# Performance work log

Measured on AMD Instinct MI355X. Metric: run time of the kernel, lower is better.

Reference implementation:

```python
import jax, jax.numpy as jnp
import numpy as np

B, Q, P, H, NH, NKV, D = 8, 16, 4096, 4096, 32, 8, 128
ROPE_BASE = 10000.0


def setup_inputs() -> dict:
    key = jax.random.key(0)
    ks = jax.random.split(key, 8)
    hidden_states = jax.random.normal(ks[0], (B, Q, H), dtype=jnp.float32)
    past_key = jax.random.normal(ks[1], (B, NKV, P, D), dtype=jnp.float32)
    past_value = jax.random.normal(ks[2], (B, NKV, P, D), dtype=jnp.float32)
    # draft tokens continue right after the cached prefix
    position_ids = jnp.broadcast_to(P + jnp.arange(Q, dtype=jnp.int64), (B, Q))
    attention_bias = jnp.zeros((B, 1, Q, P + Q), dtype=jnp.float32)
    s = 0.02
    Wq = jax.random.normal(ks[3], (H, NH * D), dtype=jnp.float32) * s
    Wk = jax.random.normal(ks[4], (H, NKV * D), dtype=jnp.float32) * s
    Wv = jax.random.normal(ks[5], (H, NKV * D), dtype=jnp.float32) * s
    Wo = jax.random.normal(ks[6], (NH * D, H), dtype=jnp.float32) * s
    return {"hidden_states": hidden_states, "position_ids": position_ids,
            "past_key": past_key, "past_value": past_value,
            "attention_bias": attention_bias, "Wq": Wq, "Wk": Wk, "Wv": Wv, "Wo": Wo}


def _rope_cos_sin(position_ids, dtype):
    # inv_freq over even dims, GPT-NeoX layout: angles repeated (concat) over halves
    inv_freq = 1.0 / (ROPE_BASE ** (jnp.arange(0, D, 2, dtype=jnp.float32) / D))
    ang = position_ids.astype(jnp.float32)[:, :, None] * inv_freq  # [B,Q,D/2]
    emb = jnp.concatenate([ang, ang], axis=-1)  # [B,Q,D]
    cos = jnp.cos(emb).astype(dtype)[:, None, :, :]  # [B,1,Q,D]
    sin = jnp.sin(emb).astype(dtype)[:, None, :, :]
    return cos, sin


def _rotate_half(x):
    x1, x2 = jnp.split(x, 2, axis=-1)
    return jnp.concatenate([-x2, x1], axis=-1)


def reference(hidden_states, position_ids, past_key, past_value, attention_bias,
              Wq, Wk, Wv, Wo):
    b, q_len, _ = hidden_states.shape
    n_kv = past_key.shape[1]
    groups = NH // n_kv
    # projections
    q = (hidden_states @ Wq).reshape(b, q_len, NH, D).transpose(0, 2, 1, 3)   # [B,NH,Q,D]
    k = (hidden_states @ Wk).reshape(b, q_len, n_kv, D).transpose(0, 2, 1, 3)  # [B,NKV,Q,D]
    v = (hidden_states @ Wv).reshape(b, q_len, n_kv, D).transpose(0, 2, 1, 3)
    # RoPE
    cos, sin = _rope_cos_sin(position_ids, hidden_states.dtype)
    q = q * cos + _rotate_half(q) * sin
    k = k * cos + _rotate_half(k) * sin
    # KV-cache append
    k_all = jnp.concatenate([past_key, k], axis=2)    # [B,NKV,S,D]
    v_all = jnp.concatenate([past_value, v], axis=2)
    # GQA attention: group query heads per kv head instead of repeat_interleave
    qg = q.reshape(b, n_kv, groups, q_len, D)
    scale = 1.0 / jnp.sqrt(jnp.asarray(D, dtype=hidden_states.dtype))
    scores = jnp.einsum('bkgqd,bksd->bkgqs', qg, k_all) * scale
    scores = scores + attention_bias[:, :, None, :, :]  # bias [B,1,Q,S] -> broadcast
    probs = jax.nn.softmax(scores, axis=-1)
    out = jnp.einsum('bkgqs,bksd->bkgqd', probs, v_all)  # [B,NKV,G,Q,D]
    out = out.reshape(b, NH, q_len, D).transpose(0, 2, 1, 3).reshape(b, q_len, NH * D)
    return out @ Wo
```

## Files before the change

### kernel.cpp

```cpp
#include <hip/hip_runtime.h>
#include <hip/hip_bf16.h>

#define NB 8
#define NQ 16
#define NP 4096
#define NHID 4096
#define NHEADS 32
#define NKVH 8
#define NG 4
#define ND 128
#define NM 128
#define NSEQ 4112
#define N_QKV 6144
#define SPLITK 8
#define NS 16

typedef __attribute__((ext_vector_type(8))) short bf16x8;
typedef __attribute__((ext_vector_type(4))) float f32x4;

__device__ __forceinline__ unsigned short f2bf(float f) {
  unsigned int u = __float_as_uint(f);
  u = (u + 0x7FFFu + ((u >> 16) & 1u)) >> 16;
  return (unsigned short)u;
}

__device__ __forceinline__ unsigned cvtpk(float lo, float hi) {
  unsigned r;
  asm("v_cvt_pk_bf16_f32 %0, %1, %2" : "=v"(r) : "v"(lo), "v"(hi));
  return r;
}

__device__ __forceinline__ float bf2f(unsigned short u) {
  return __uint_as_float(((unsigned)u) << 16);
}

#define TRREAD(dst, a32) \
  asm volatile("ds_read_b64_tr_b16 %0, %1" : "=v"(dst) : "v"(a32))
#define LGKM0() asm volatile("s_waitcnt lgkmcnt(0)" ::: "memory")
#define SBAR()                              \
  do {                                      \
    __builtin_amdgcn_sched_barrier(0);      \
    __builtin_amdgcn_s_barrier();           \
    __builtin_amdgcn_sched_barrier(0);      \
  } while (0)

__global__ __launch_bounds__(256) void k_cvt(const float* __restrict__ x,
                                             unsigned short* __restrict__ y, int n4) {
  int i = blockIdx.x * 256 + threadIdx.x;
  if (i >= n4) return;
  f32x4 v = ((const f32x4*)x)[i];
  uint2 o;
  o.x = cvtpk(v[0], v[1]);
  o.y = cvtpk(v[2], v[3]);
  ((uint2*)y)[i] = o;
}

template<int CT>
__global__ __launch_bounds__(256) void k_gemm(
    const unsigned short* __restrict__ A, int lda,
    const float* __restrict__ W0, const float* __restrict__ W1,
    const float* __restrict__ W2, int nw0, int nw1, int N, int KS,
    float* __restrict__ part) {
  constexpr int BN = CT * 32;
  constexpr int NT = CT * 2;
  constexpr int NW4 = BN / 4;
  constexpr int KST = 256 / NW4;
  __shared__ __align__(16) char Bl[8 * NT * 128];
  int n0 = blockIdx.x * BN;
  int k0 = blockIdx.y * KS;
  const float* Wp; int ldw, ncol;
  if (n0 < nw0)      { Wp = W0; ldw = nw0;       ncol = n0; }
  else if (n0 < nw1) { Wp = W1; ldw = nw1 - nw0; ncol = n0 - nw0; }
  else               { Wp = W2; ldw = N - nw1;   ncol = n0 - nw1; }
  int tid = threadIdx.x, lane = tid & 63, wid = tid >> 6;
  int r16 = lane & 15, hi = lane >> 4;
  int wr = wid >> 1, wc = wid & 1;
  int n4 = tid & (NW4 - 1), krow = tid / NW4;
  unsigned lb = (unsigned)(uintptr_t)(void*)Bl;

  f32x4 acc[4][CT];
#pragma unroll
  for (int i = 0; i < 4; ++i)
#pragma unroll
    for (int j = 0; j < CT; ++j) acc[i][j] = {0.f, 0.f, 0.f, 0.f};

  f32x4 cur[CT], nxt[CT];
#pragma unroll
  for (int r = 0; r < CT; ++r) {
    cur[r] = *(const f32x4*)&Wp[(size_t)(k0 + krow + r * KST) * ldw + ncol + n4 * 4];
    nxt[r] = cur[r];
  }

  for (int kk = 0; kk < KS; kk += 32) {
    SBAR();
    if (kk + 32 < KS) {
#pragma unroll
      for (int r = 0; r < CT; ++r)
        nxt[r] = *(const f32x4*)&Wp[(size_t)(k0 + kk + 32 + krow + r * KST) * ldw + ncol + n4 * 4];
    }
#pragma unroll
    for (int r = 0; r < CT; ++r) {
      int k = krow + r * KST;
      uint2 u;
      u.x = cvtpk(cur[r][0], cur[r][1]);
      u.y = cvtpk(cur[r][2], cur[r][3]);
      *(uint2*)(Bl + ((k >> 2) * NT + (n4 >> 2)) * 128 + (k & 3) * 32 + (n4 & 3) * 8) = u;
    }
    LGKM0();
    SBAR();
    bf16x8 af[4];
#pragma unroll
    for (int rt = 0; rt < 4; ++rt)
      af[rt] = *(const bf16x8*)&A[(size_t)(wr * 64 + rt * 16 + r16) * lda + k0 + kk + hi * 8];
    unsigned long long rr[2 * CT];
#pragma unroll
    for (int ct = 0; ct < CT; ++ct) {
      int s1 = hi * (2 * NT) + wc * CT + ct;
      TRREAD(rr[ct * 2],     lb + s1 * 128 + r16 * 8);
      TRREAD(rr[ct * 2 + 1], lb + (s1 + NT) * 128 + r16 * 8);
    }
    LGKM0();
    __builtin_amdgcn_sched_barrier(0);
    __builtin_amdgcn_s_setprio(1);
#pragma unroll
    for (int ct = 0; ct < CT; ++ct) {
      union { unsigned long long u[2]; bf16x8 v; } cc;
      cc.u[0] = rr[ct * 2]; cc.u[1] = rr[ct * 2 + 1];
#pragma unroll
      for (int rt = 0; rt < 4; ++rt)
        acc[rt][ct] = __builtin_amdgcn_mfma_f32_16x16x32_bf16(af[rt], cc.v, acc[rt][ct], 0, 0, 0);
    }
    __builtin_amdgcn_s_setprio(0);
#pragma unroll
    for (int r = 0; r < CT; ++r) cur[r] = nxt[r];
  }
  float* po = part + (size_t)blockIdx.y * NM * N;
#pragma unroll
  for (int rt = 0; rt < 4; ++rt)
#pragma unroll
    for (int ct = 0; ct < CT; ++ct)
#pragma unroll
      for (int r = 0; r < 4; ++r) {
        int m = wr * 64 + rt * 16 + hi * 4 + r;
        int n = n0 + wc * CT * 16 + ct * 16 + r16;
        po[(size_t)m * N + n] = acc[rt][ct][r];
      }
}

__global__ __launch_bounds__(256) void k_rope(
    const float* __restrict__ part, const void* __restrict__ posv,
    unsigned short* __restrict__ qb, unsigned short* __restrict__ kb,
    unsigned short* __restrict__ vb) {
  int t = blockIdx.x * 256 + threadIdx.x;
  int d = t & 63;
  int rest = t >> 6;
  int h = rest % 48;
  int m = rest / 48;
  if (m >= NM) return;
  const int* p32 = (const int*)posv;
  const long long* p64 = (const long long*)posv;
  bool is64 = (p64[0] == (long long)p32[0]);
  int pos = is64 ? (int)p64[m] : p32[m];
  int b = m >> 4, q = m & 15;

  int c1, c2;
  if (h < 32)      { c1 = h * ND + d; }
  else if (h < 40) { c1 = NHID + (h - 32) * ND + d; }
  else             { c1 = NHID + 1024 + (h - 40) * ND + d; }
  c2 = c1 + 64;
  float x1 = 0.f, x2 = 0.f;
#pragma unroll
  for (int c = 0; c < SPLITK; ++c) {
    x1 += part[((size_t)c * NM + m) * N_QKV + c1];
    x2 += part[((size_t)c * NM + m) * N_QKV + c2];
  }
  if (h < 40) {
    float invf = __expf(-(float)d * 0.14391156831212787f);
    float th = (float)pos * invf;
    float cs = cosf(th), sn = sinf(th);
    float o1 = x1 * cs - x2 * sn;
    float o2 = x2 * cs + x1 * sn;
    if (h < 32) {
      o1 *= 0.08838834764831845f;
      o2 *= 0.08838834764831845f;
      int kv = h >> 2, g = h & 3;
      size_t base = ((((size_t)b * NKVH + kv) * NG + g) * NQ + q) * ND;
      qb[base + d] = f2bf(o1);
      qb[base + d + 64] = f2bf(o2);
    } else {
      int kvh = h - 32;
      size_t base = (((size_t)b * NKVH + kvh) * NQ + q) * ND;
      kb[base + d] = f2bf(o1);
      kb[base + d + 64] = f2bf(o2);
    }
  } else {
    int kvh = h - 40;
    size_t base = (((size_t)b * NKVH + kvh) * NQ + q) * ND;
    vb[base + d] = f2bf(x1);
    vb[base + d + 64] = f2bf(x2);
  }
}

template<int NSPL>
__global__ __launch_bounds__(256, 2) void k_attn(
    const unsigned short* __restrict__ qb, const unsigned short* __restrict__ kb,
    const unsigned short* __restrict__ vb, const float* __restrict__ pastK,
    const float* __restrict__ pastV, const float* __restrict__ bias,
    unsigned short* __restrict__ pout, float* __restrict__ pml) {
  __shared__ __align__(16) char lds[40960];
  char* Pl = lds + 32768;
  constexpr int KEYS = NP / NSPL;
  constexpr int NSUB = KEYS / 32;
  int bkv = blockIdx.x;
  int split = blockIdx.y;
  int b = bkv >> 3, kv = bkv & 7;
  int tid = threadIdx.x, lane = tid & 63, wid = tid >> 6;
  int r16 = lane & 15, hi = lane >> 4;

  const unsigned short* qbase = qb + ((((size_t)b * NKVH + kv) * NG + wid) * NQ) * ND;
  bf16x8 qf[4];
#pragma unroll
  for (int kd = 0; kd < 4; ++kd)
    qf[kd] = *(const bf16x8*)&qbase[r16 * ND + kd * 32 + hi * 8];

  float m_run[4], l_lane[4];
  f32x4 oacc[8];
#pragma unroll
  for (int r = 0; r < 4; ++r) { m_run[r] = -1e30f; l_lane[r] = 0.f; }
#pragma unroll
  for (int dt = 0; dt < 8; ++dt) oacc[dt] = {0.f, 0.f, 0.f, 0.f};

  int s0 = split * KEYS;
  const float* Kg = pastK + ((size_t)(b * NKVH + kv) * NP + s0) * ND;
  const float* Vg = pastV + ((size_t)(b * NKVH + kv) * NP + s0) * ND;
  const float* biasrow = bias + (size_t)(b * NQ) * NSEQ;
  int d4 = tid & 31, sr = tid >> 5;
  bool last = (split == NSPL - 1);

  f32x4 rwK[4], rwV[4];
  float br0, br1, bt[4];
  bf16x8 tk, tv;

  auto kissue = [&](int tile) {
    const float* Kn = Kg + (size_t)tile * 32 * ND;
#pragma unroll
    for (int it = 0; it < 4; ++it)
      rwK[it] = *(const f32x4*)&Kn[(size_t)(sr + it * 8) * ND + d4 * 4];
  };
  auto vissue = [&](int tile) {
    const float* Vn = Vg + (size_t)tile * 32 * ND;
#pragma unroll
    for (int it = 0; it < 4; ++it)
      rwV[it] = *(const f32x4*)&Vn[(size_t)(sr + it * 8) * ND + d4 * 4];
  };
  auto bissue = [&](int tile) {
    {
      int e = tid;        int q = e >> 5, j = e & 31;
      br0 = biasrow[(size_t)q * NSEQ + s0 + tile * 32 + j];
    }
    {
      int e = 256 + tid;  int q = e >> 5, j = e & 31;
      br1 = biasrow[(size_t)q * NSEQ + s0 + tile * 32 + j];
    }
  };
  auto kconv = [&](char* Kl) {
#pragma unroll
    for (int it = 0; it < 4; ++it) {
      int s = sr + it * 8;
      uint2 u;
      u.x = cvtpk(rwK[it][0], rwK[it][1]); u.y = cvtpk(rwK[it][2], rwK[it][3]);
      *(uint2*)(Kl + s * 256 + ((d4 * 8) ^ ((s & 7) << 4))) = u;
    }
  };
  auto vconv = [&](char* Vl) {
#pragma unroll
    for (int it = 0; it < 4; ++it) {
      int s = sr + it * 8;
      uint2 u;
      u.x = cvtpk(rwV[it][0], rwV[it][1]); u.y = cvtpk(rwV[it][2], rwV[it][3]);
      *(uint2*)(Vl + ((s >> 2) * 8 + (d4 >> 2)) * 128 + (s & 3) * 32 + (d4 & 3) * 8) = u;
    }
  };
  auto bstore = [&](char* Bb) {
    {
      int e = tid;        int q = e >> 5, j = e & 31;
      *(float*)(Bb + q * 128 + ((j * 4) ^ ((q & 7) << 4))) = br0;
    }
    {
      int e = 256 + tid;  int q = e >> 5, j = e & 31;
      *(float*)(Bb + q * 128 + ((j * 4) ^ ((q & 7) << 4))) = br1;
    }
  };

  f32x4 sc[2];
  auto qk_softmax = [&](char* Kl, char* Bb, bool tail) {
    __builtin_amdgcn_s_setprio(1);
#pragma unroll
    for (int ct = 0; ct < 2; ++ct) {
      f32x4 a = {0.f, 0.f, 0.f, 0.f};
      int s = ct * 16 + r16;
#pragma unroll
      for (int kd = 0; kd < 4; ++kd) {
        bf16x8 kf = *(const bf16x8*)(Kl + s * 256 + ((kd * 64 + hi * 16) ^ ((s & 7) << 4)));
        a = __builtin_amdgcn_mfma_f32_16x16x32_bf16(qf[kd], kf, a, 0, 0, 0);
      }
      sc[ct] = a;
    }
    __builtin_amdgcn_s_setprio(0);
    if (!tail) {
#pragma unroll
      for (int ct = 0; ct < 2; ++ct)
#pragma unroll
        for (int r = 0; r < 4; ++r) {
          int q = hi * 4 + r, j = ct * 16 + r16;
          sc[ct][r] += *(const float*)(Bb + q * 128 + ((j * 4) ^ ((q & 7) << 4)));
        }
    } else {
#pragma unroll
      for (int ct = 0; ct < 2; ++ct)
#pragma unroll
        for (int r = 0; r < 4; ++r) {
          if (ct == 0) sc[ct][r] += bt[r];
          else         sc[ct][r] = -1e30f;
        }
    }
    float pmax[4];
#pragma unroll
    for (int r = 0; r < 4; ++r)
      pmax[r] = fmaxf(sc[0][r], sc[1][r]);
    bool ok = (pmax[0] <= m_run[0] + 8.f) && (pmax[1] <= m_run[1] + 8.f) &&
              (pmax[2] <= m_run[2] + 8.f) && (pmax[3] <= m_run[3] + 8.f);
    if (!__all(ok)) {
#pragma unroll
      for (int r = 0; r < 4; ++r) {
        float v = pmax[r];
        v = fmaxf(v, __shfl_xor(v, 1));
        v = fmaxf(v, __shfl_xor(v, 2));
        v = fmaxf(v, __shfl_xor(v, 4));
        v = fmaxf(v, __shfl_xor(v, 8));
        float mnew = fmaxf(m_run[r], v);
        float fac = __expf(m_run[r] - mnew);
        m_run[r] = mnew;
        l_lane[r] *= fac;
#pragma unroll
        for (int dt = 0; dt < 8; ++dt) oacc[dt][r] *= fac;
      }
    }
#pragma unroll
    for (int ct = 0; ct < 2; ++ct)
#pragma unroll
      for (int r = 0; r < 4; ++r) {
        float p = __expf(sc[ct][r] - m_run[r]);
        l_lane[r] += p;
        int q = hi * 4 + r, j2 = ct * 16 + r16;
        *(unsigned short*)(Pl + wid * 1024 + q * 64 + ((j2 * 2) ^ ((q & 3) << 4))) = f2bf(p);
      }
  };

  auto pv = [&](char* Vl) {
    unsigned vb32 = (unsigned)(uintptr_t)(void*)Vl;
    bf16x8 pa = *(const bf16x8*)(Pl + wid * 1024 + r16 * 64 +
                                 ((hi * 16) ^ ((r16 & 3) << 4)));
#pragma unroll
    for (int dh = 0; dh < 2; ++dh) {
      unsigned long long rr[8];
#pragma unroll
      for (int dq = 0; dq < 4; ++dq) {
        int sA = hi * 16 + dh * 4 + dq;
        TRREAD(rr[dq * 2],     vb32 + sA * 128 + r16 * 8);
        TRREAD(rr[dq * 2 + 1], vb32 + (sA + 8) * 128 + r16 * 8);
      }
      LGKM0();
      __builtin_amdgcn_sched_barrier(0);
      __builtin_amdgcn_s_setprio(1);
#pragma unroll
      for (int dq = 0; dq < 4; ++dq) {
        union { unsigned long long u[2]; bf16x8 v; } cc;
        cc.u[0] = rr[dq * 2]; cc.u[1] = rr[dq * 2 + 1];
        oacc[dh * 4 + dq] = __builtin_amdgcn_mfma_f32_16x16x32_bf16(pa, cc.v, oacc[dh * 4 + dq], 0, 0, 0);
      }
      __builtin_amdgcn_s_setprio(0);
    }
  };

  kissue(0);
  vissue(0);
  bissue(0);
  kconv(lds + 0);
  vconv(lds + 16384);
  bstore(lds + 36864);
  LGKM0();

  int cur = 0;
  for (int sub = 0; sub < NSUB; ++sub) {
    char* KlC = lds + cur * 8192;
    char* VlC = lds + 16384 + cur * 8192;
    char* BbC = lds + 36864 + cur * 2048;
    char* KlN = lds + (cur ^ 1) * 8192;
    char* VlN = lds + 16384 + (cur ^ 1) * 8192;
    char* BbN = lds + 36864 + (cur ^ 1) * 2048;
    SBAR();
    bool pf = (sub + 1 < NSUB);
    if (pf) {
      kissue(sub + 1);
      bissue(sub + 1);
    } else if (last) {
      int s = tid >> 4, d8 = tid & 15;
      const unsigned short* Kn = kb + (((size_t)b * NKVH + kv) * NQ) * ND;
      const unsigned short* Vn = vb + (((size_t)b * NKVH + kv) * NQ) * ND;
      tk = *(const bf16x8*)&Kn[s * ND + d8 * 8];
      tv = *(const bf16x8*)&Vn[s * ND + d8 * 8];
#pragma unroll
      for (int r = 0; r < 4; ++r)
        bt[r] = biasrow[(size_t)(hi * 4 + r) * NSEQ + NP + r16];
    }
    qk_softmax(KlC, BbC, false);
    if (pf) {
      kconv(KlN);
      vissue(sub + 1);
    } else if (last) {
      int s = tid >> 4, d8 = tid & 15;
      *(bf16x8*)(KlN + s * 256 + ((d8 * 16) ^ ((s & 7) << 4))) = tk;
    }
    pv(VlC);
    if (pf) {
      vconv(VlN);
      bstore(BbN);
    } else if (last) {
      int s = tid >> 4, d8 = tid & 15;
      *(bf16x8*)(VlN + ((s >> 2) * 8 + (d8 >> 1)) * 128 + (s & 3) * 32 + (d8 & 1) * 16) = tv;
    }
    LGKM0();
    if (pf || last) cur ^= 1;
  }
  if (last) {
    SBAR();
    qk_softmax(lds + cur * 8192, (char*)0, true);
    pv(lds + 16384 + cur * 8192);
  }

  float l_run[4];
#pragma unroll
  for (int r = 0; r < 4; ++r) {
    float s = l_lane[r];
    s += __shfl_xor(s, 1);
    s += __shfl_xor(s, 2);
    s += __shfl_xor(s, 4);
    s += __shfl_xor(s, 8);
    l_run[r] = s;
  }
  SBAR();
  char* My = lds + wid * 4096;
#pragma unroll
  for (int dt = 0; dt < 8; ++dt)
#pragma unroll
    for (int r = 0; r < 4; ++r)
      *(unsigned short*)(My + (hi * 4 + r) * 256 + (dt * 16 + r16) * 2) = f2bf(oacc[dt][r]);
  LGKM0();
  const int NROW = NB * NKVH * NG * NQ;
  size_t rowbase = ((size_t)(b * NKVH + kv) * NG + wid) * NQ;
  unsigned short* po = pout + ((size_t)split * NROW + rowbase) * ND;
#pragma unroll
  for (int it = 0; it < 4; ++it) {
    int row = it * 4 + (lane >> 4);
    uint4 vv = *(uint4*)(My + row * 256 + r16 * 16);
    *(uint4*)&po[(size_t)row * ND + r16 * 8] = vv;
  }
  if (r16 == 0) {
#pragma unroll
    for (int r = 0; r < 4; ++r) {
      size_t idx = ((size_t)split * NROW + rowbase + hi * 4 + r) * 2;
      pml[idx] = m_run[r];
      pml[idx + 1] = l_run[r];
    }
  }
}

template<int NSPL>
__global__ __launch_bounds__(256) void k_combine(
    const unsigned short* __restrict__ pout, const float* __restrict__ pml,
    unsigned short* __restrict__ Aatt) {
  const int NROW = NB * NKVH * NG * NQ;
  int row = blockIdx.x * 2 + (threadIdx.x >> 7);
  int d = threadIdx.x & 127;
  float mv[NSPL], lv[NSPL];
  float M = -1e30f;
#pragma unroll
  for (int c = 0; c < NSPL; ++c) {
    mv[c] = pml[((size_t)c * NROW + row) * 2];
    lv[c] = pml[((size_t)c * NROW + row) * 2 + 1];
    M = fmaxf(M, mv[c]);
  }
  float L = 0.f, acc = 0.f;
#pragma unroll
  for (int c = 0; c < NSPL; ++c) {
    float w = __expf(mv[c] - M);
    L += lv[c] * w;
    acc += bf2f(pout[((size_t)c * NROW + row) * ND + d]) * w;
  }
  float o = acc / L;
  int q = row & 15, g = (row >> 4) & 3, kvh = (row >> 6) & 7, b = row >> 9;
  Aatt[(size_t)(b * NQ + q) * NHID + (kvh * NG + g) * ND + d] = f2bf(o);
}

__global__ __launch_bounds__(256) void k_red(const float* __restrict__ part,
                                             float* __restrict__ out) {
  int i = blockIdx.x * 256 + threadIdx.x;
  float s = 0.f;
#pragma unroll
  for (int c = 0; c < SPLITK; ++c) s += part[(size_t)c * (NM * NHID) + i];
  out[i] = s;
}

extern "C" void kernel_launch(void* const* d_in, const int* in_sizes, int n_in,
                              void* d_out, int out_size, void* d_ws, size_t ws_size,
                              hipStream_t stream) {
  const float* hidden = (const float*)d_in[0];
  const void* pos = d_in[1];
  const float* pastK = (const float*)d_in[2];
  const float* pastV = (const float*)d_in[3];
  const float* bias = (const float*)d_in[4];
  const float* Wq = (const float*)d_in[5];
  const float* Wk = (const float*)d_in[6];
  const float* Wv = (const float*)d_in[7];
  const float* Wo = (const float*)d_in[8];
  float* out = (float*)d_out;

  char* ws = (char*)d_ws;
  size_t off = 0;
  auto alloc = [&](size_t bytes) {
    char* p = ws + off;
    off += (bytes + 255) & ~(size_t)255;
    return p;
  };
  unsigned short* hb   = (unsigned short*)alloc((size_t)NM * NHID * 2);
  unsigned short* qb   = (unsigned short*)alloc((size_t)NB * NKVH * NG * NQ * ND * 2);
  unsigned short* kb   = (unsigned short*)alloc((size_t)NB * NKVH * NQ * ND * 2);
  unsigned short* vb   = (unsigned short*)alloc((size_t)NB * NKVH * NQ * ND * 2);
  unsigned short* Aatt = (unsigned short*)alloc((size_t)NM * NHID * 2);

  size_t ml16 = (size_t)16 * 8192 * 2 * 4;
  size_t po16 = (size_t)16 * 8192 * ND * 2;
  size_t partB = (size_t)SPLITK * NM * N_QKV * 4;
  size_t need16 = (ml16 + po16 > partB) ? ml16 + po16 : partB;
  int NSP = (ws_size >= off + need16 + 4096) ? 16 : 8;
  float* pml = (float*)(ws + off);
  unsigned short* pout = (unsigned short*)(ws + off + (NSP == 16 ? ml16 : ml16 / 2));
  float* part = (float*)(ws + off);

  k_cvt<<<512, 256, 0, stream>>>(hidden, hb, NM * NHID / 4);
  k_gemm<2><<<dim3(96, SPLITK), 256, 0, stream>>>(hb, NHID, Wq, Wk, Wv, 4096, 5120,
                                                  N_QKV, NHID / SPLITK, part);
  k_rope<<<1536, 256, 0, stream>>>(part, pos, qb, kb, vb);
  if (NSP == 16) {
    k_attn<16><<<dim3(64, 16), 256, 0, stream>>>(qb, kb, vb, pastK, pastV, bias, pout, pml);
    k_combine<16><<<4096, 256, 0, stream>>>(pout, pml, Aatt);
  } else {
    k_attn<8><<<dim3(64, 8), 256, 0, stream>>>(qb, kb, vb, pastK, pastV, bias, pout, pml);
    k_combine<8><<<4096, 256, 0, stream>>>(pout, pml, Aatt);
  }
  k_gemm<2><<<dim3(64, SPLITK), 256, 0, stream>>>(Aatt, NHID, Wo, Wo, Wo, 4096, 8192,
                                                  NHID, NHID / SPLITK, part);
  k_red<<<2048, 256, 0, stream>>>(part, out);
}
```

Baseline: 154.2 us.

## Prefetch K and bias two tiles ahead with ping-pong register sets

K tiles and bias rows are now loaded into global-memory registers two sub-tiles ahead, alternating between two register sets (A/B). V loads are issued at the start of each iteration, which gives them more time to land before conversion. The loop is fully unrolled so the buffer parity is a compile-time constant. This aims to hide more global-load latency, at the cost of extra VGPRs that may reduce occupancy.

```diff
diff --git a/kernel.cpp b/kernel.cpp
--- a/kernel.cpp
+++ b/kernel.cpp
@@ -13,7 +13,6 @@
 #define NSEQ 4112
 #define N_QKV 6144
 #define SPLITK 8
-#define NS 16
 
 typedef __attribute__((ext_vector_type(8))) short bf16x8;
 typedef __attribute__((ext_vector_type(4))) float f32x4;
@@ -237,59 +236,78 @@
   int d4 = tid & 31, sr = tid >> 5;
   bool last = (split == NSPL - 1);
 
-  f32x4 rwK[4], rwV[4];
-  float br0, br1, bt[4];
+  f32x4 kRA[4], kRB[4], vR[4];
+  float brA0, brA1, brB0, brB1, bt[4];
   bf16x8 tk, tv;
 
-  auto kissue = [&](int tile) {
+  auto kissueA = [&](int tile) {
     const float* Kn = Kg + (size_t)tile * 32 * ND;
 #pragma unroll
     for (int it = 0; it < 4; ++it)
-      rwK[it] = *(const f32x4*)&Kn[(size_t)(sr + it * 8) * ND + d4 * 4];
+      kRA[it] = *(const f32x4*)&Kn[(size_t)(sr + it * 8) * ND + d4 * 4];
+  };
+  auto kissueB = [&](int tile) {
+    const float* Kn = Kg + (size_t)tile * 32 * ND;
+#pragma unroll
+    for (int it = 0; it < 4; ++it)
+      kRB[it] = *(const f32x4*)&Kn[(size_t)(sr + it * 8) * ND + d4 * 4];
   };
   auto vissue = [&](int tile) {
     const float* Vn = Vg + (size_t)tile * 32 * ND;
 #pragma unroll
     for (int it = 0; it < 4; ++it)
-      rwV[it] = *(const f32x4*)&Vn[(size_t)(sr + it * 8) * ND + d4 * 4];
-  };
-  auto bissue = [&](int tile) {
-    {
-      int e = tid;        int q = e >> 5, j = e & 31;
-      br0 = biasrow[(size_t)q * NSEQ + s0 + tile * 32 + j];
-    }
-    {
-      int e = 256 + tid;  int q = e >> 5, j = e & 31;
-      br1 = biasrow[(size_t)q * NSEQ + s0 + tile * 32 + j];
-    }
-  };
-  auto kconv = [&](char* Kl) {
+      vR[it] = *(const f32x4*)&Vn[(size_t)(sr + it * 8) * ND + d4 * 4];
+  };
+  auto bissueA = [&](int tile) {
+    { int e = tid;       int q = e >> 5, j = e & 31;
+      brA0 = biasrow[(size_t)q * NSEQ + s0 + tile * 32 + j]; }
+    { int e = 256 + tid; int q = e >> 5, j = e & 31;
+      brA1 = biasrow[(size_t)q * NSEQ + s0 + tile * 32 + j]; }
+  };
+  auto bissueB = [&](int tile) {
+    { int e = tid;       int q = e >> 5, j = e & 31;
+      brB0 = biasrow[(size_t)q * NSEQ + s0 + tile * 32 + j]; }
+    { int e = 256 + tid; int q = e >> 5, j = e & 31;
+      brB1 = biasrow[(size_t)q * NSEQ + s0 + tile * 32 + j]; }
+  };
+  auto kconvA = [&](char* Kl) {
 #pragma unroll
     for (int it = 0; it < 4; ++it) {
       int s = sr + it * 8;
       uint2 u;
-      u.x = cvtpk(rwK[it][0], rwK[it][1]); u.y = cvtpk(rwK[it][2], rwK[it][3]);
+      u.x = cvtpk(kRA[it][0], kRA[it][1]); u.y = cvtpk(kRA[it][2], kRA[it][3]);
       *(uint2*)(Kl + s * 256 + ((d4 * 8) ^ ((s & 7) << 4))) = u;
     }
   };
-  auto vconv = [&](char* Vl) {
+  auto kconvB = [&](char* Kl) {
 #pragma unroll
     for (int it = 0; it < 4; ++it) {
       int s = sr + it * 8;
       uint2 u;
-      u.x = cvtpk(rwV[it][0], rwV[it][1]); u.y = cvtpk(rwV[it][2], rwV[it][3]);
+      u.x = cvtpk(kRB[it][0], kRB[it][1]); u.y = cvtpk(kRB[it][2], kRB[it][3]);
+      *(uint2*)(Kl + s * 256 + ((d4 * 8) ^ ((s & 7) << 4))) = u;
+    }
+  };
+  auto vconv = [&](char* Vl) {
+#pragma unroll
+    for (int it = 0; it < 4; ++it) {
+      int s = sr + it * 8;
+      uint2 u;
+      u.x = cvtpk(vR[it][0], vR[it][1]); u.y = cvtpk(vR[it][2], vR[it][3]);
       *(uint2*)(Vl + ((s >> 2) * 8 + (d4 >> 2)) * 128 + (s & 3) * 32 + (d4 & 3) * 8) = u;
     }
   };
-  auto bstore = [&](char* Bb) {
-    {
-      int e = tid;        int q = e >> 5, j = e & 31;
-      *(float*)(Bb + q * 128 + ((j * 4) ^ ((q & 7) << 4))) = br0;
-    }
-    {
-      int e = 256 + tid;  int q = e >> 5, j = e & 31;
-      *(float*)(Bb + q * 128 + ((j * 4) ^ ((q & 7) << 4))) = br1;
-    }
+  auto bstoreA = [&](char* Bb) {
+    { int e = tid;       int q = e >> 5, j = e & 31;
+      *(float*)(Bb + q * 128 + ((j * 4) ^ ((q & 7) << 4))) = brA0; }
+    { int e = 256 + tid; int q = e >> 5, j = e & 31;
+      *(float*)(Bb + q * 128 + ((j * 4) ^ ((q & 7) << 4))) = brA1; }
+  };
+  auto bstoreB = [&](char* Bb) {
+    { int e = tid;       int q = e >> 5, j = e & 31;
+      *(float*)(Bb + q * 128 + ((j * 4) ^ ((q & 7) << 4))) = brB0; }
+    { int e = 256 + tid; int q = e >> 5, j = e & 31;
+      *(float*)(Bb + q * 128 + ((j * 4) ^ ((q & 7) << 4))) = brB1; }
   };
 
   f32x4 sc[2];
@@ -383,28 +401,31 @@
     }
   };
 
-  kissue(0);
+  kissueA(0);
   vissue(0);
-  bissue(0);
-  kconv(lds + 0);
+  bissueA(0);
+  kissueB(1);
+  bissueB(1);
+  kconvA(lds + 0);
   vconv(lds + 16384);
-  bstore(lds + 36864);
+  bstoreA(lds + 36864);
   LGKM0();
 
-  int cur = 0;
+#pragma unroll
   for (int sub = 0; sub < NSUB; ++sub) {
-    char* KlC = lds + cur * 8192;
-    char* VlC = lds + 16384 + cur * 8192;
-    char* BbC = lds + 36864 + cur * 2048;
-    char* KlN = lds + (cur ^ 1) * 8192;
-    char* VlN = lds + 16384 + (cur ^ 1) * 8192;
-    char* BbN = lds + 36864 + (cur ^ 1) * 2048;
+    const int p = sub & 1;
+    char* KlC = lds + p * 8192;
+    char* VlC = lds + 16384 + p * 8192;
+    char* BbC = lds + 36864 + p * 2048;
+    char* KlN = lds + (p ^ 1) * 8192;
+    char* VlN = lds + 16384 + (p ^ 1) * 8192;
+    char* BbN = lds + 36864 + (p ^ 1) * 2048;
     SBAR();
-    bool pf = (sub + 1 < NSUB);
-    if (pf) {
-      kissue(sub + 1);
-      bissue(sub + 1);
-    } else if (last) {
+    if (sub + 1 < NSUB) vissue(sub + 1);
+    if (sub + 2 < NSUB) {
+      if (p == 0) { kissueA(sub + 2); bissueA(sub + 2); }
+      else        { kissueB(sub + 2); bissueB(sub + 2); }
+    } else if (sub + 2 == NSUB && last) {
       int s = tid >> 4, d8 = tid & 15;
       const unsigned short* Kn = kb + (((size_t)b * NKVH + kv) * NQ) * ND;
       const unsigned short* Vn = vb + (((size_t)b * NKVH + kv) * NQ) * ND;
@@ -415,28 +436,26 @@
         bt[r] = biasrow[(size_t)(hi * 4 + r) * NSEQ + NP + r16];
     }
     qk_softmax(KlC, BbC, false);
-    if (pf) {
-      kconv(KlN);
-      vissue(sub + 1);
+    if (sub + 1 < NSUB) {
+      if (p == 0) { kconvB(KlN); bstoreB(BbN); }
+      else        { kconvA(KlN); bstoreA(BbN); }
     } else if (last) {
       int s = tid >> 4, d8 = tid & 15;
       *(bf16x8*)(KlN + s * 256 + ((d8 * 16) ^ ((s & 7) << 4))) = tk;
     }
     pv(VlC);
-    if (pf) {
+    if (sub + 1 < NSUB) {
       vconv(VlN);
-      bstore(BbN);
     } else if (last) {
       int s = tid >> 4, d8 = tid & 15;
       *(bf16x8*)(VlN + ((s >> 2) * 8 + (d8 >> 1)) * 128 + (s & 3) * 32 + (d8 & 1) * 16) = tv;
     }
     LGKM0();
-    if (pf || last) cur ^= 1;
   }
   if (last) {
     SBAR();
-    qk_softmax(lds + cur * 8192, (char*)0, true);
-    pv(lds + 16384 + cur * 8192);
+    qk_softmax(lds + (NSUB & 1) * 8192, (char*)0, true);
+    pv(lds + 16384 + (NSUB & 1) * 8192);
   }
 
   float l_run[4];
```

Measured after the change: 154.6 us. Within noise of the previous version (+0.2%).

## Rework attention so each wave owns a private key range without block barriers

Applied to the files above, without the earlier changes.

The split-KV attention kernel is rebuilt. Each block now serves one query group, and each of its four waves walks its own slice of keys with private LDS buffers for K, V and P, so no block-wide barriers are needed. Bias is loaded straight into registers instead of being staged through LDS. The split count drops to 4 (or 2), giving 16 (or 8) partial slots per row, which matches the existing combine kernel. The cost is that each fp32 K/V tile is now fetched by four blocks (one per group) instead of once per block, so more global or L2 traffic and more registers per wave are traded for removing synchronisation.

```diff
diff --git a/kernel.cpp b/kernel.cpp
--- a/kernel.cpp
+++ b/kernel.cpp
@@ -13,7 +13,6 @@
 #define NSEQ 4112
 #define N_QKV 6144
 #define SPLITK 8
-#define NS 16
 
 typedef __attribute__((ext_vector_type(8))) short bf16x8;
 typedef __attribute__((ext_vector_type(4))) float f32x4;
@@ -202,22 +201,27 @@
 }
 
 template<int NSPL>
-__global__ __launch_bounds__(256, 2) void k_attn(
+__global__ __launch_bounds__(256) void k_attn3(
     const unsigned short* __restrict__ qb, const unsigned short* __restrict__ kb,
     const unsigned short* __restrict__ vb, const float* __restrict__ pastK,
     const float* __restrict__ pastV, const float* __restrict__ bias,
     unsigned short* __restrict__ pout, float* __restrict__ pml) {
-  __shared__ __align__(16) char lds[40960];
-  char* Pl = lds + 32768;
-  constexpr int KEYS = NP / NSPL;
-  constexpr int NSUB = KEYS / 32;
-  int bkv = blockIdx.x;
+  __shared__ __align__(16) char lds[69632];
+  constexpr int RK = NP / NSPL / 4;
+  constexpr int ITER = RK / 32;
+  int g = blockIdx.x & 3, bkv = blockIdx.x >> 2;
   int split = blockIdx.y;
   int b = bkv >> 3, kv = bkv & 7;
   int tid = threadIdx.x, lane = tid & 63, wid = tid >> 6;
   int r16 = lane & 15, hi = lane >> 4;
-
-  const unsigned short* qbase = qb + ((((size_t)b * NKVH + kv) * NG + wid) * NQ) * ND;
+  int lrow = lane >> 2, lq = lane & 3;
+  char* S  = lds + wid * 17408;
+  char* Kl = S;
+  char* Vl = S + 8192;
+  char* Pb = S + 16384;
+  bool tailw = (split == NSPL - 1) && (wid == 3);
+
+  const unsigned short* qbase = qb + ((((size_t)b * NKVH + kv) * NG + g) * NQ) * ND;
   bf16x8 qf[4];
 #pragma unroll
   for (int kd = 0; kd < 4; ++kd)
@@ -230,70 +234,84 @@
 #pragma unroll
   for (int dt = 0; dt < 8; ++dt) oacc[dt] = {0.f, 0.f, 0.f, 0.f};
 
-  int s0 = split * KEYS;
+  int s0 = split * (NP / NSPL) + wid * RK;
   const float* Kg = pastK + ((size_t)(b * NKVH + kv) * NP + s0) * ND;
   const float* Vg = pastV + ((size_t)(b * NKVH + kv) * NP + s0) * ND;
   const float* biasrow = bias + (size_t)(b * NQ) * NSEQ;
-  int d4 = tid & 31, sr = tid >> 5;
-  bool last = (split == NSPL - 1);
-
-  f32x4 rwK[4], rwV[4];
-  float br0, br1, bt[4];
-  bf16x8 tk, tv;
-
-  auto kissue = [&](int tile) {
-    const float* Kn = Kg + (size_t)tile * 32 * ND;
-#pragma unroll
-    for (int it = 0; it < 4; ++it)
-      rwK[it] = *(const f32x4*)&Kn[(size_t)(sr + it * 8) * ND + d4 * 4];
-  };
-  auto vissue = [&](int tile) {
-    const float* Vn = Vg + (size_t)tile * 32 * ND;
-#pragma unroll
-    for (int it = 0; it < 4; ++it)
-      rwV[it] = *(const f32x4*)&Vn[(size_t)(sr + it * 8) * ND + d4 * 4];
-  };
-  auto bissue = [&](int tile) {
-    {
-      int e = tid;        int q = e >> 5, j = e & 31;
-      br0 = biasrow[(size_t)q * NSEQ + s0 + tile * 32 + j];
-    }
-    {
-      int e = 256 + tid;  int q = e >> 5, j = e & 31;
-      br1 = biasrow[(size_t)q * NSEQ + s0 + tile * 32 + j];
-    }
-  };
-  auto kconv = [&](char* Kl) {
-#pragma unroll
-    for (int it = 0; it < 4; ++it) {
-      int s = sr + it * 8;
+
+  f32x4 kLo[8], kHi[8], vLo[8], vHi[8];
+  float br[8], bt[4] = {0.f, 0.f, 0.f, 0.f};
+
+  auto kisL = [&](int t) {
+    const float* P = Kg + (size_t)t * 32 * ND;
+#pragma unroll
+    for (int i = 0; i < 8; ++i)
+      kLo[i] = *(const f32x4*)&P[(size_t)lrow * ND + lq * 32 + i * 4];
+  };
+  auto kisH = [&](int t) {
+    const float* P = Kg + ((size_t)t * 32 + 16) * ND;
+#pragma unroll
+    for (int i = 0; i < 8; ++i)
+      kHi[i] = *(const f32x4*)&P[(size_t)lrow * ND + lq * 32 + i * 4];
+  };
+  auto visL = [&](int t) {
+    const float* P = Vg + (size_t)t * 32 * ND;
+#pragma unroll
+    for (int i = 0; i < 8; ++i)
+      vLo[i] = *(const f32x4*)&P[(size_t)lrow * ND + lq * 32 + i * 4];
+  };
+  auto visH = [&](int t) {
+    const float* P = Vg + ((size_t)t * 32 + 16) * ND;
+#pragma unroll
+    for (int i = 0; i < 8; ++i)
+      vHi[i] = *(const f32x4*)&P[(size_t)lrow * ND + lq * 32 + i * 4];
+  };
+  auto bis = [&](int t) {
+#pragma unroll
+    for (int ct = 0; ct < 2; ++ct)
+#pragma unroll
+      for (int r = 0; r < 4; ++r)
+        br[ct * 4 + r] = biasrow[(size_t)(hi * 4 + r) * NSEQ + s0 + t * 32 + ct * 16 + r16];
+  };
+  auto kcvL = [&]() {
+#pragma unroll
+    for (int i = 0; i < 8; ++i) {
+      int s = lrow, d0 = lq * 32 + i * 4;
       uint2 u;
-      u.x = cvtpk(rwK[it][0], rwK[it][1]); u.y = cvtpk(rwK[it][2], rwK[it][3]);
-      *(uint2*)(Kl + s * 256 + ((d4 * 8) ^ ((s & 7) << 4))) = u;
-    }
-  };
-  auto vconv = [&](char* Vl) {
-#pragma unroll
-    for (int it = 0; it < 4; ++it) {
-      int s = sr + it * 8;
+      u.x = cvtpk(kLo[i][0], kLo[i][1]); u.y = cvtpk(kLo[i][2], kLo[i][3]);
+      *(uint2*)(Kl + s * 256 + ((d0 * 2) ^ ((s & 7) << 4))) = u;
+    }
+  };
+  auto kcvH = [&]() {
+#pragma unroll
+    for (int i = 0; i < 8; ++i) {
+      int s = lrow + 16, d0 = lq * 32 + i * 4;
       uint2 u;
-      u.x = cvtpk(rwV[it][0], rwV[it][1]); u.y = cvtpk(rwV[it][2], rwV[it][3]);
-      *(uint2*)(Vl + ((s >> 2) * 8 + (d4 >> 2)) * 128 + (s & 3) * 32 + (d4 & 3) * 8) = u;
-    }
-  };
-  auto bstore = [&](char* Bb) {
-    {
-      int e = tid;        int q = e >> 5, j = e & 31;
-      *(float*)(Bb + q * 128 + ((j * 4) ^ ((q & 7) << 4))) = br0;
-    }
-    {
-      int e = 256 + tid;  int q = e >> 5, j = e & 31;
-      *(float*)(Bb + q * 128 + ((j * 4) ^ ((q & 7) << 4))) = br1;
+      u.x = cvtpk(kHi[i][0], kHi[i][1]); u.y = cvtpk(kHi[i][2], kHi[i][3]);
+      *(uint2*)(Kl + s * 256 + ((d0 * 2) ^ ((s & 7) << 4))) = u;
+    }
+  };
+  auto vcvL = [&]() {
+#pragma unroll
+    for (int i = 0; i < 8; ++i) {
+      int s = lrow, d0 = lq * 32 + i * 4;
+      uint2 u;
+      u.x = cvtpk(vLo[i][0], vLo[i][1]); u.y = cvtpk(vLo[i][2], vLo[i][3]);
+      *(uint2*)(Vl + ((s >> 2) * 8 + (d0 >> 4)) * 128 + (s & 3) * 32 + (d0 & 15) * 2) = u;
+    }
+  };
+  auto vcvH = [&]() {
+#pragma unroll
+    for (int i = 0; i < 8; ++i) {
+      int s = lrow + 16, d0 = lq * 32 + i * 4;
+      uint2 u;
+      u.x = cvtpk(vHi[i][0], vHi[i][1]); u.y = cvtpk(vHi[i][2], vHi[i][3]);
+      *(uint2*)(Vl + ((s >> 2) * 8 + (d0 >> 4)) * 128 + (s & 3) * 32 + (d0 & 15) * 2) = u;
     }
   };
 
   f32x4 sc[2];
-  auto qk_softmax = [&](char* Kl, char* Bb, bool tail) {
+  auto qk_softmax = [&](bool tail) {
     __builtin_amdgcn_s_setprio(1);
 #pragma unroll
     for (int ct = 0; ct < 2; ++ct) {
@@ -311,10 +329,8 @@
 #pragma unroll
       for (int ct = 0; ct < 2; ++ct)
 #pragma unroll
-        for (int r = 0; r < 4; ++r) {
-          int q = hi * 4 + r, j = ct * 16 + r16;
-          sc[ct][r] += *(const float*)(Bb + q * 128 + ((j * 4) ^ ((q & 7) << 4)));
-        }
+        for (int r = 0; r < 4; ++r)
+          sc[ct][r] += br[ct * 4 + r];
     } else {
 #pragma unroll
       for (int ct = 0; ct < 2; ++ct)
@@ -353,14 +369,13 @@
         float p = __expf(sc[ct][r] - m_run[r]);
         l_lane[r] += p;
         int q = hi * 4 + r, j2 = ct * 16 + r16;
-        *(unsigned short*)(Pl + wid * 1024 + q * 64 + ((j2 * 2) ^ ((q & 3) << 4))) = f2bf(p);
-      }
-  };
-
-  auto pv = [&](char* Vl) {
+        *(unsigned short*)(Pb + q * 64 + ((j2 * 2) ^ ((q & 3) << 4))) = f2bf(p);
+      }
+  };
+
+  auto pv = [&]() {
     unsigned vb32 = (unsigned)(uintptr_t)(void*)Vl;
-    bf16x8 pa = *(const bf16x8*)(Pl + wid * 1024 + r16 * 64 +
-                                 ((hi * 16) ^ ((r16 & 3) << 4)));
+    bf16x8 pa = *(const bf16x8*)(Pb + r16 * 64 + ((hi * 16) ^ ((r16 & 3) << 4)));
 #pragma unroll
     for (int dh = 0; dh < 2; ++dh) {
       unsigned long long rr[8];
@@ -383,60 +398,41 @@
     }
   };
 
-  kissue(0);
-  vissue(0);
-  bissue(0);
-  kconv(lds + 0);
-  vconv(lds + 16384);
-  bstore(lds + 36864);
+  kisL(0); kisH(0); visL(0); visH(0);
+  bis(0);
+  kcvL(); kcvH(); vcvL(); vcvH();
   LGKM0();
 
-  int cur = 0;
-  for (int sub = 0; sub < NSUB; ++sub) {
-    char* KlC = lds + cur * 8192;
-    char* VlC = lds + 16384 + cur * 8192;
-    char* BbC = lds + 36864 + cur * 2048;
-    char* KlN = lds + (cur ^ 1) * 8192;
-    char* VlN = lds + 16384 + (cur ^ 1) * 8192;
-    char* BbN = lds + 36864 + (cur ^ 1) * 2048;
-    SBAR();
-    bool pf = (sub + 1 < NSUB);
-    if (pf) {
-      kissue(sub + 1);
-      bissue(sub + 1);
-    } else if (last) {
-      int s = tid >> 4, d8 = tid & 15;
+  for (int t = 0; t < ITER; ++t) {
+    bool pf = (t + 1 < ITER);
+    if (pf) { kisL(t + 1); kisH(t + 1); visL(t + 1); visH(t + 1); }
+    qk_softmax(false);
+    if (pf) bis(t + 1);
+    if (pf) { kcvL(); kcvH(); }
+    pv();
+    if (pf) { vcvL(); vcvH(); }
+    else if (tailw) {
       const unsigned short* Kn = kb + (((size_t)b * NKVH + kv) * NQ) * ND;
       const unsigned short* Vn = vb + (((size_t)b * NKVH + kv) * NQ) * ND;
-      tk = *(const bf16x8*)&Kn[s * ND + d8 * 8];
-      tv = *(const bf16x8*)&Vn[s * ND + d8 * 8];
+#pragma unroll
+      for (int i = 0; i < 4; ++i) {
+        bf16x8 kk = *(const bf16x8*)&Kn[(size_t)lrow * ND + lq * 32 + i * 8];
+        int db = lq * 64 + i * 16;
+        *(bf16x8*)(Kl + lrow * 256 + (db ^ ((lrow & 7) << 4))) = kk;
+        bf16x8 vv = *(const bf16x8*)&Vn[(size_t)lrow * ND + lq * 32 + i * 8];
+        int d0 = lq * 32 + i * 8;
+        *(bf16x8*)(Vl + ((lrow >> 2) * 8 + (d0 >> 4)) * 128 +
+                   (lrow & 3) * 32 + (d0 & 15) * 2) = vv;
+      }
 #pragma unroll
       for (int r = 0; r < 4; ++r)
         bt[r] = biasrow[(size_t)(hi * 4 + r) * NSEQ + NP + r16];
     }
-    qk_softmax(KlC, BbC, false);
-    if (pf) {
-      kconv(KlN);
-      vissue(sub + 1);
-    } else if (last) {
-      int s = tid >> 4, d8 = tid & 15;
-      *(bf16x8*)(KlN + s * 256 + ((d8 * 16) ^ ((s & 7) << 4))) = tk;
-    }
-    pv(VlC);
-    if (pf) {
-      vconv(VlN);
-      bstore(BbN);
-    } else if (last) {
-      int s = tid >> 4, d8 = tid & 15;
-      *(bf16x8*)(VlN + ((s >> 2) * 8 + (d8 >> 1)) * 128 + (s & 3) * 32 + (d8 & 1) * 16) = tv;
-    }
     LGKM0();
-    if (pf || last) cur ^= 1;
-  }
-  if (last) {
-    SBAR();
-    qk_softmax(lds + cur * 8192, (char*)0, true);
-    pv(lds + 16384 + cur * 8192);
+  }
+  if (tailw) {
+    qk_softmax(true);
+    pv();
   }
 
   float l_run[4];
@@ -449,8 +445,7 @@
     s += __shfl_xor(s, 8);
     l_run[r] = s;
   }
-  SBAR();
-  char* My = lds + wid * 4096;
+  char* My = Kl;
 #pragma unroll
   for (int dt = 0; dt < 8; ++dt)
 #pragma unroll
@@ -458,18 +453,19 @@
       *(unsigned short*)(My + (hi * 4 + r) * 256 + (dt * 16 + r16) * 2) = f2bf(oacc[dt][r]);
   LGKM0();
   const int NROW = NB * NKVH * NG * NQ;
-  size_t rowbase = ((size_t)(b * NKVH + kv) * NG + wid) * NQ;
-  unsigned short* po = pout + ((size_t)split * NROW + rowbase) * ND;
+  int slot = split * 4 + wid;
+  size_t rowbase = ((size_t)(b * NKVH + kv) * NG + g) * NQ;
+  unsigned short* po = pout + ((size_t)slot * NROW + rowbase) * ND;
 #pragma unroll
   for (int it = 0; it < 4; ++it) {
-    int row = it * 4 + (lane >> 4);
+    int row = it * 4 + hi;
     uint4 vv = *(uint4*)(My + row * 256 + r16 * 16);
     *(uint4*)&po[(size_t)row * ND + r16 * 8] = vv;
   }
   if (r16 == 0) {
 #pragma unroll
     for (int r = 0; r < 4; ++r) {
-      size_t idx = ((size_t)split * NROW + rowbase + hi * 4 + r) * 2;
+      size_t idx = ((size_t)slot * NROW + rowbase + hi * 4 + r) * 2;
       pml[idx] = m_run[r];
       pml[idx + 1] = l_run[r];
     }
@@ -543,20 +539,20 @@
   size_t po16 = (size_t)16 * 8192 * ND * 2;
   size_t partB = (size_t)SPLITK * NM * N_QKV * 4;
   size_t need16 = (ml16 + po16 > partB) ? ml16 + po16 : partB;
-  int NSP = (ws_size >= off + need16 + 4096) ? 16 : 8;
+  int NSP = (ws_size >= off + need16 + 4096) ? 4 : 2;
   float* pml = (float*)(ws + off);
-  unsigned short* pout = (unsigned short*)(ws + off + (NSP == 16 ? ml16 : ml16 / 2));
+  unsigned short* pout = (unsigned short*)(ws + off + (NSP == 4 ? ml16 : ml16 / 2));
   float* part = (float*)(ws + off);
 
   k_cvt<<<512, 256, 0, stream>>>(hidden, hb, NM * NHID / 4);
   k_gemm<2><<<dim3(96, SPLITK), 256, 0, stream>>>(hb, NHID, Wq, Wk, Wv, 4096, 5120,
                                                   N_QKV, NHID / SPLITK, part);
   k_rope<<<1536, 256, 0, stream>>>(part, pos, qb, kb, vb);
-  if (NSP == 16) {
-    k_attn<16><<<dim3(64, 16), 256, 0, stream>>>(qb, kb, vb, pastK, pastV, bias, pout, pml);
+  if (NSP == 4) {
+    k_attn3<4><<<dim3(256, 4), 256, 0, stream>>>(qb, kb, vb, pastK, pastV, bias, pout, pml);
     k_combine<16><<<4096, 256, 0, stream>>>(pout, pml, Aatt);
   } else {
-    k_attn<8><<<dim3(64, 8), 256, 0, stream>>>(qb, kb, vb, pastK, pastV, bias, pout, pml);
+    k_attn3<2><<<dim3(256, 2), 256, 0, stream>>>(qb, kb, vb, pastK, pastV, bias, pout, pml);
     k_combine<8><<<4096, 256, 0, stream>>>(pout, pml, Aatt);
   }
   k_gemm<2><<<dim3(64, SPLITK), 256, 0, stream>>>(Aatt, NHID, Wo, Wo, Wo, 4096, 8192,
```

Measured after the change: 269.4 us. 74.7% more time.

## Double-buffer LDS weight tiles with 64-wide K steps in split-K GEMM

Applied to the files above, without the earlier changes.

Restructures the split-K GEMM main loop to use two LDS buffers and a K-step of 64 instead of 32. Global weight loads run two tiles ahead and the bf16 conversion store goes into the alternate buffer while MFMAs consume the current one. This drops one barrier per iteration and overlaps LDS writes with compute. In exchange it doubles LDS use per block and fixes the per-thread load count at 4 regardless of CT, which is only correct when KST*4 equals 64, so CT values other than 2 could produce wrong results.

```diff
diff --git a/kernel.cpp b/kernel.cpp
--- a/kernel.cpp
+++ b/kernel.cpp
@@ -13,7 +13,6 @@
 #define NSEQ 4112
 #define N_QKV 6144
 #define SPLITK 8
-#define NS 16
 
 typedef __attribute__((ext_vector_type(8))) short bf16x8;
 typedef __attribute__((ext_vector_type(4))) float f32x4;
@@ -65,7 +64,8 @@
   constexpr int NT = CT * 2;
   constexpr int NW4 = BN / 4;
   constexpr int KST = 256 / NW4;
-  __shared__ __align__(16) char Bl[8 * NT * 128];
+  constexpr int BUF = 16 * NT * 128;
+  __shared__ __align__(16) char Bl[2 * BUF];
   int n0 = blockIdx.x * BN;
   int k0 = blockIdx.y * KS;
   const float* Wp; int ldw, ncol;
@@ -76,7 +76,6 @@
   int r16 = lane & 15, hi = lane >> 4;
   int wr = wid >> 1, wc = wid & 1;
   int n4 = tid & (NW4 - 1), krow = tid / NW4;
-  unsigned lb = (unsigned)(uintptr_t)(void*)Bl;
 
   f32x4 acc[4][CT];
 #pragma unroll
@@ -84,55 +83,69 @@
 #pragma unroll
     for (int j = 0; j < CT; ++j) acc[i][j] = {0.f, 0.f, 0.f, 0.f};
 
-  f32x4 cur[CT], nxt[CT];
-#pragma unroll
-  for (int r = 0; r < CT; ++r) {
-    cur[r] = *(const f32x4*)&Wp[(size_t)(k0 + krow + r * KST) * ldw + ncol + n4 * 4];
-    nxt[r] = cur[r];
-  }
-
-  for (int kk = 0; kk < KS; kk += 32) {
-    SBAR();
-    if (kk + 32 < KS) {
-#pragma unroll
-      for (int r = 0; r < CT; ++r)
-        nxt[r] = *(const f32x4*)&Wp[(size_t)(k0 + kk + 32 + krow + r * KST) * ldw + ncol + n4 * 4];
-    }
-#pragma unroll
-    for (int r = 0; r < CT; ++r) {
+  f32x4 cur[4];
+  auto wissue = [&](int t) {
+#pragma unroll
+    for (int r = 0; r < 4; ++r)
+      cur[r] = *(const f32x4*)&Wp[(size_t)(k0 + t * 64 + krow + r * KST) * ldw + ncol + n4 * 4];
+  };
+  auto wstore = [&](char* buf) {
+#pragma unroll
+    for (int r = 0; r < 4; ++r) {
       int k = krow + r * KST;
       uint2 u;
       u.x = cvtpk(cur[r][0], cur[r][1]);
       u.y = cvtpk(cur[r][2], cur[r][3]);
-      *(uint2*)(Bl + ((k >> 2) * NT + (n4 >> 2)) * 128 + (k & 3) * 32 + (n4 & 3) * 8) = u;
+      *(uint2*)(buf + ((k >> 2) * NT + (n4 >> 2)) * 128 + (k & 3) * 32 + (n4 & 3) * 8) = u;
+    }
+  };
+
+  const int NTK = KS / 64;
+  wissue(0);
+  wstore(Bl);
+  wissue(1);
+  LGKM0();
+  SBAR();
+
+  int p = 0;
+  for (int t = 0; t < NTK; ++t) {
+    char* bufC = Bl + p * BUF;
+    char* bufN = Bl + (p ^ 1) * BUF;
+    if (t + 1 < NTK) {
+      wstore(bufN);
+      if (t + 2 < NTK) wissue(t + 2);
+    }
+#pragma unroll
+    for (int h = 0; h < 2; ++h) {
+      bf16x8 af[4];
+#pragma unroll
+      for (int rt = 0; rt < 4; ++rt)
+        af[rt] = *(const bf16x8*)&A[(size_t)(wr * 64 + rt * 16 + r16) * lda +
+                                    k0 + t * 64 + h * 32 + hi * 8];
+      unsigned long long rr[2 * CT];
+      unsigned cb = (unsigned)(uintptr_t)(void*)bufC;
+#pragma unroll
+      for (int ct = 0; ct < CT; ++ct) {
+        int s1 = h * 8 * NT + hi * (2 * NT) + wc * CT + ct;
+        TRREAD(rr[ct * 2],     cb + s1 * 128 + r16 * 8);
+        TRREAD(rr[ct * 2 + 1], cb + (s1 + NT) * 128 + r16 * 8);
+      }
+      LGKM0();
+      __builtin_amdgcn_sched_barrier(0);
+      __builtin_amdgcn_s_setprio(1);
+#pragma unroll
+      for (int ct = 0; ct < CT; ++ct) {
+        union { unsigned long long u[2]; bf16x8 v; } cc;
+        cc.u[0] = rr[ct * 2]; cc.u[1] = rr[ct * 2 + 1];
+#pragma unroll
+        for (int rt = 0; rt < 4; ++rt)
+          acc[rt][ct] = __builtin_amdgcn_mfma_f32_16x16x32_bf16(af[rt], cc.v, acc[rt][ct], 0, 0, 0);
+      }
+      __builtin_amdgcn_s_setprio(0);
     }
     LGKM0();
-    SBAR();
-    bf16x8 af[4];
-#pragma unroll
-    for (int rt = 0; rt < 4; ++rt)
-      af[rt] = *(const bf16x8*)&A[(size_t)(wr * 64 + rt * 16 + r16) * lda + k0 + kk + hi * 8];
-    unsigned long long rr[2 * CT];
-#pragma unroll
-    for (int ct = 0; ct < CT; ++ct) {
-      int s1 = hi * (2 * NT) + wc * CT + ct;
-      TRREAD(rr[ct * 2],     lb + s1 * 128 + r16 * 8);
-      TRREAD(rr[ct * 2 + 1], lb + (s1 + NT) * 128 + r16 * 8);
-    }
-    LGKM0();
-    __builtin_amdgcn_sched_barrier(0);
-    __builtin_amdgcn_s_setprio(1);
-#pragma unroll
-    for (int ct = 0; ct < CT; ++ct) {
-      union { unsigned long long u[2]; bf16x8 v; } cc;
-      cc.u[0] = rr[ct * 2]; cc.u[1] = rr[ct * 2 + 1];
-#pragma unroll
-      for (int rt = 0; rt < 4; ++rt)
-        acc[rt][ct] = __builtin_amdgcn_mfma_f32_16x16x32_bf16(af[rt], cc.v, acc[rt][ct], 0, 0, 0);
-    }
-    __builtin_amdgcn_s_setprio(0);
-#pragma unroll
-    for (int r = 0; r < CT; ++r) cur[r] = nxt[r];
+    if (t + 1 < NTK) SBAR();
+    p ^= 1;
   }
   float* po = part + (size_t)blockIdx.y * NM * N;
 #pragma unroll
```

Result: no change. 156.8 us (+1.7%).
